# Kernel tuning notes

Hardware: AMD Instinct MI355X
Metric: run time of the kernel (lower is better)

Reference implementation:

```python
import jax, jax.numpy as jnp
import numpy as np

T, H, I, E, K = 2048, 2048, 1408, 8, 2


def setup_inputs() -> dict:
    key = jax.random.key(0)
    k1, k2, k3, k4, k5 = jax.random.split(key, 5)
    s_h = 1.0 / np.sqrt(H)
    s_i = 1.0 / np.sqrt(I)
    return {
        "hidden_states": jax.random.normal(k1, (T, H), dtype=jnp.float32),
        "router_logits": jax.random.normal(k2, (T, E), dtype=jnp.float32),
        "Wg": jax.random.normal(k3, (E, H, I), dtype=jnp.float32) * s_h,
        "Wu": jax.random.normal(k4, (E, H, I), dtype=jnp.float32) * s_h,
        "Wd": jax.random.normal(k5, (E, I, H), dtype=jnp.float32) * s_i,
        "top_k": K,
    }


def reference(hidden_states, router_logits, Wg, Wu, Wd, top_k):
    # top-k routing: softmax over the selected top-k logits (as in torch.topk + softmax)
    topk_vals, topk_ids = jax.lax.top_k(router_logits, top_k)  # [T,K]
    topk_w = jax.nn.softmax(topk_vals, axis=-1)                # [T,K]

    n_tok = hidden_states.shape[0]
    n_exp = router_logits.shape[-1]
    # combine weights [T,E]: scatter top-k weights back to expert slots
    cw = jnp.zeros((n_tok, n_exp), hidden_states.dtype)
    cw = cw.at[jnp.arange(n_tok)[:, None], topk_ids].add(topk_w)

    out = jnp.zeros_like(hidden_states)
    for e in range(n_exp):  # small fixed expert count
        g = hidden_states @ Wg[e]          # [T,I]
        u = hidden_states @ Wu[e]          # [T,I]
        y = (jax.nn.silu(g) * u) @ Wd[e]   # [T,H]
        out = out + cw[:, e:e + 1] * y
    return out
```

## Files before the change

### kernel.cpp

```cpp
#include <hip/hip_runtime.h>
#include <hip/hip_bf16.h>
#include <cstdint>
#include <cstddef>

#define TT 2048
#define HH 2048
#define II 1408
#define EE 8
#define MAXROWS 5120

typedef unsigned short u16;
typedef __attribute__((ext_vector_type(8))) __bf16 bf16x8;
typedef __attribute__((ext_vector_type(4))) float f32x4;

typedef const __attribute__((address_space(1))) uint32_t* gas1_t;
typedef __attribute__((address_space(3))) uint32_t* las3_t;

__device__ __forceinline__ float bf2f(u16 b) {
    return __uint_as_float(((uint32_t)b) << 16);
}
__device__ __forceinline__ u16 f2bf(float x) {
    uint32_t u = __float_as_uint(x);
    u += 0x7fffu + ((u >> 16) & 1u);
    return (u16)(u >> 16);
}

__global__ void k_sniff(const u16* __restrict__ raw, int* __restrict__ flag) {
    __shared__ int cnt;
    if (threadIdx.x == 0) cnt = 0;
    __syncthreads();
    int w = 0;
    for (int i = threadIdx.x; i < 4096; i += 256) {
        u16 x = raw[i];
        if (x & 0x7fff) {
            int ex = (x >> 7) & 0xff;
            if (ex == 0xff || ex < 100 || ex > 140) ++w;
        }
    }
    atomicAdd(&cnt, w);
    __syncthreads();
    if (threadIdx.x == 0) flag[0] = (cnt > 100) ? 1 : 0;
}

__global__ void k_zero(float* __restrict__ out_acc, int* __restrict__ counts) {
    const int i0 = (blockIdx.x * 256 + threadIdx.x) * 4;
    *(float4*)&out_acc[i0] = make_float4(0.f, 0.f, 0.f, 0.f);
    if (blockIdx.x == 0 && threadIdx.x < EE) counts[threadIdx.x] = 0;
}

__global__ void k_routing2(const void* __restrict__ logits, const int* __restrict__ flag,
                           int* __restrict__ counts, int* __restrict__ idx,
                           float* __restrict__ wt) {
    int t = blockIdx.x * 256 + threadIdx.x;
    if (t >= TT) return;
    const int f = flag[0];
    float v[EE];
#pragma unroll
    for (int e = 0; e < EE; ++e)
        v[e] = f ? ((const float*)logits)[t * EE + e]
                 : bf2f(((const u16*)logits)[t * EE + e]);
    int i0 = 0; float v0 = v[0];
#pragma unroll
    for (int e = 1; e < EE; ++e) { if (v[e] > v0) { v0 = v[e]; i0 = e; } }
    int i1 = -1; float v1 = -3.4e38f;
#pragma unroll
    for (int e = 0; e < EE; ++e) { if (e != i0 && v[e] > v1) { v1 = v[e]; i1 = e; } }
    float r = __expf(v1 - v0);
    float s = 1.f / (1.f + r);
    int p0 = atomicAdd(&counts[i0], 1);
    idx[i0 * TT + p0] = t; wt[i0 * TT + p0] = s;
    int p1 = atomicAdd(&counts[i1], 1);
    idx[i1 * TT + p1] = t; wt[i1 * TT + p1] = r * s;
}

__global__ void k_offsets(const int* __restrict__ counts, int* __restrict__ meta) {
    if (threadIdx.x == 0 && blockIdx.x == 0) {
        int off = 0;
        for (int e = 0; e < EE; ++e) {
            int c = counts[e];
            int p = (c + 127) & ~127;
            meta[e] = off; meta[8 + e] = p;
            off += p;
        }
    }
}

__global__ void k_cast(const void* __restrict__ src, const int* __restrict__ flag,
                       u16* __restrict__ dst) {
    const int i0 = (blockIdx.x * 256 + threadIdx.x) * 8;
    if (flag[0]) {
        const float* s = (const float*)src;
#pragma unroll
        for (int j = 0; j < 8; ++j) dst[i0 + j] = f2bf(s[i0 + j]);
    } else {
        const u16* s = (const u16*)src;
        *(uint4*)&dst[i0] = *(const uint4*)&s[i0];
    }
}

__global__ void k_transposeV(const void* __restrict__ src, const int* __restrict__ flag,
                             u16* __restrict__ dst, int R, int C) {
    __shared__ u16 t[64][68];
    const size_t eo = (size_t)blockIdx.z * (size_t)R * (size_t)C;
    const int r0 = blockIdx.y * 64, c0 = blockIdx.x * 64;
    const int tid = threadIdx.x;
    const int f = flag[0];
    {
        const int cg = tid & 15, rr = tid >> 4;
#pragma unroll
        for (int p = 0; p < 4; ++p) {
            const int r = rr + p * 16;
            const size_t base = eo + (size_t)(r0 + r) * C + c0 + cg * 4;
            if (f) {
                const float4 v = *(const float4*)((const float*)src + base);
                t[r][cg * 4 + 0] = f2bf(v.x); t[r][cg * 4 + 1] = f2bf(v.y);
                t[r][cg * 4 + 2] = f2bf(v.z); t[r][cg * 4 + 3] = f2bf(v.w);
            } else {
                const ushort4 v = *(const ushort4*)((const u16*)src + base);
                t[r][cg * 4 + 0] = v.x; t[r][cg * 4 + 1] = v.y;
                t[r][cg * 4 + 2] = v.z; t[r][cg * 4 + 3] = v.w;
            }
        }
    }
    __syncthreads();
    {
        const int rg = tid & 15, cc = tid >> 4;
#pragma unroll
        for (int p = 0; p < 4; ++p) {
            const int c = cc + p * 16;
            ushort4 o;
            o.x = t[rg * 4 + 0][c]; o.y = t[rg * 4 + 1][c];
            o.z = t[rg * 4 + 2][c]; o.w = t[rg * 4 + 3][c];
            *(ushort4*)(dst + eo + (size_t)(c0 + c) * R + r0 + rg * 4) = o;
        }
    }
}

__device__ __forceinline__ void stage16(const u16* __restrict__ g, int stride_elems,
                                        u16* lds, int wave, int lane) {
    const int sub = lane >> 2;
    const int col = (lane & 3) * 8;
#pragma unroll
    for (int h = 0; h < 2; ++h) {
        const int rbase = wave * 32 + h * 16;
        const u16* ga = g + (size_t)(rbase + sub) * stride_elems + col;
        __builtin_amdgcn_global_load_lds((gas1_t)ga, (las3_t)(lds + rbase * 32), 16, 0, 0);
    }
}

__global__ __launch_bounds__(256, 2)
void k_gemm1s(const u16* __restrict__ hs_b,
              const u16* __restrict__ Wgt,
              const u16* __restrict__ Wut,
              const int* __restrict__ counts,
              const int* __restrict__ meta,
              const int* __restrict__ idx,
              const float* __restrict__ wt,
              u16* __restrict__ act_g) {
    const int e = blockIdx.z;
    const int cnt = counts[e];
    const int pcnt = meta[8 + e];
    const int m0 = blockIdx.y * 128;
    if (m0 >= pcnt) return;
    const int n0 = blockIdx.x * 128;
    const int off = meta[e];
    const int tid = threadIdx.x;
    const int wave = tid >> 6, lane = tid & 63;
    const int ln = lane & 15, q = lane >> 4;
    const int wr = (wave >> 1) * 64, wc = (wave & 1) * 64;

    __shared__ __align__(16) u16 As[128 * 32];
    __shared__ __align__(16) u16 Bg[128 * 32];
    __shared__ __align__(16) u16 Bu[128 * 32];
    __shared__ int   tokS[128];
    __shared__ float wtS[128];

    if (tid < 128) {
        const int pos = m0 + tid;
        const bool v = pos < cnt;
        tokS[tid] = v ? idx[e * TT + pos] : 0;
        wtS[tid]  = v ? wt[e * TT + pos] : 0.f;
    }
    __syncthreads();

    const int sub = lane >> 2, col = (lane & 3) * 8;
    const int r0 = wave * 32 + sub;
    const u16* pA0 = hs_b + (size_t)tokS[r0] * HH + col;
    const u16* pA1 = hs_b + (size_t)tokS[r0 + 16] * HH + col;
    const u16* gG = Wgt + ((size_t)e * II + n0) * HH;
    const u16* gU = Wut + ((size_t)e * II + n0) * HH;

    f32x4 accg[4][4], accu[4][4];
#pragma unroll
    for (int mi = 0; mi < 4; ++mi)
#pragma unroll
        for (int ni = 0; ni < 4; ++ni) { accg[mi][ni] = (f32x4)0.f; accu[mi][ni] = (f32x4)0.f; }

    for (int kb = 0; kb < HH; kb += 32) {
        __syncthreads();
        __builtin_amdgcn_global_load_lds((gas1_t)(pA0 + kb), (las3_t)(As + (wave * 32) * 32), 16, 0, 0);
        __builtin_amdgcn_global_load_lds((gas1_t)(pA1 + kb), (las3_t)(As + (wave * 32 + 16) * 32), 16, 0, 0);
        stage16(gG + kb, HH, Bg, wave, lane);
        stage16(gU + kb, HH, Bu, wave, lane);
        __syncthreads();

        bf16x8 af[4];
#pragma unroll
        for (int mi = 0; mi < 4; ++mi)
            af[mi] = *(const bf16x8*)&As[(wr + mi * 16 + ln) * 32 + q * 8];
#pragma unroll
        for (int ni = 0; ni < 4; ++ni) {
            bf16x8 bgf = *(const bf16x8*)&Bg[(wc + ni * 16 + ln) * 32 + q * 8];
            bf16x8 buf = *(const bf16x8*)&Bu[(wc + ni * 16 + ln) * 32 + q * 8];
#pragma unroll
            for (int mi = 0; mi < 4; ++mi) {
                accg[mi][ni] = __builtin_amdgcn_mfma_f32_16x16x32_bf16(af[mi], bgf, accg[mi][ni], 0, 0, 0);
                accu[mi][ni] = __builtin_amdgcn_mfma_f32_16x16x32_bf16(af[mi], buf, accu[mi][ni], 0, 0, 0);
            }
        }
    }

#pragma unroll
    for (int mi = 0; mi < 4; ++mi) {
#pragma unroll
        for (int r = 0; r < 4; ++r) {
            const int row = wr + mi * 16 + q * 4 + r;
            const float w = wtS[row];
#pragma unroll
            for (int ni = 0; ni < 4; ++ni) {
                const int i = n0 + wc + ni * 16 + ln;
                const float g = accg[mi][ni][r];
                const float u = accu[mi][ni][r];
                const float y = w * u * g / (1.f + __expf(-g));
                act_g[(size_t)(off + m0 + row) * II + i] = f2bf(y);
            }
        }
    }
}

__global__ __launch_bounds__(256, 2)
void k_gemm2s(const u16* __restrict__ act_g,
              const u16* __restrict__ Wdt,
              const int* __restrict__ counts,
              const int* __restrict__ meta,
              const int* __restrict__ idx,
              float* __restrict__ out_acc) {
    const int e = blockIdx.z;
    const int cnt = counts[e];
    const int pcnt = meta[8 + e];
    const int m0 = blockIdx.y * 128;
    if (m0 >= pcnt) return;
    const int n0 = blockIdx.x * 128;
    const int off = meta[e];
    const int tid = threadIdx.x;
    const int wave = tid >> 6, lane = tid & 63;
    const int ln = lane & 15, q = lane >> 4;
    const int wr = (wave >> 1) * 64, wc = (wave & 1) * 64;

    __shared__ __align__(16) u16 As[128 * 32];
    __shared__ __align__(16) u16 Bs[128 * 32];
    __shared__ int tokS[128];

    if (tid < 128) {
        const int pos = m0 + tid;
        tokS[tid] = (pos < cnt) ? idx[e * TT + pos] : -1;
    }

    const u16* bA = act_g + (size_t)(off + m0) * II;
    const u16* bB = Wdt + ((size_t)e * HH + n0) * II;

    f32x4 acc[4][4];
#pragma unroll
    for (int mi = 0; mi < 4; ++mi)
#pragma unroll
        for (int ni = 0; ni < 4; ++ni) acc[mi][ni] = (f32x4)0.f;

    for (int i0 = 0; i0 < II; i0 += 32) {
        __syncthreads();
        stage16(bA + i0, II, As, wave, lane);
        stage16(bB + i0, II, Bs, wave, lane);
        __syncthreads();

        bf16x8 af[4];
#pragma unroll
        for (int mi = 0; mi < 4; ++mi)
            af[mi] = *(const bf16x8*)&As[(wr + mi * 16 + ln) * 32 + q * 8];
#pragma unroll
        for (int ni = 0; ni < 4; ++ni) {
            bf16x8 bf = *(const bf16x8*)&Bs[(wc + ni * 16 + ln) * 32 + q * 8];
#pragma unroll
            for (int mi = 0; mi < 4; ++mi)
                acc[mi][ni] = __builtin_amdgcn_mfma_f32_16x16x32_bf16(af[mi], bf, acc[mi][ni], 0, 0, 0);
        }
    }

#pragma unroll
    for (int mi = 0; mi < 4; ++mi) {
#pragma unroll
        for (int r = 0; r < 4; ++r) {
            const int row = wr + mi * 16 + q * 4 + r;
            const int t = tokS[row];
            if (t >= 0) {
#pragma unroll
                for (int ni = 0; ni < 4; ++ni) {
                    const int h = n0 + wc + ni * 16 + ln;
                    unsafeAtomicAdd(&out_acc[(size_t)t * HH + h], acc[mi][ni][r]);
                }
            }
        }
    }
}

__global__ void k_out(const float* __restrict__ out_acc, const int* __restrict__ flag,
                      void* __restrict__ out) {
    const int i0 = (blockIdx.x * 256 + threadIdx.x) * 4;
    const float4 v = *(const float4*)&out_acc[i0];
    if (flag[0]) {
        *(float4*)((float*)out + i0) = v;
    } else {
        u16* o = (u16*)out + i0;
        o[0] = f2bf(v.x); o[1] = f2bf(v.y); o[2] = f2bf(v.z); o[3] = f2bf(v.w);
    }
}

extern "C" void kernel_launch(void* const* d_in, const int* in_sizes, int n_in,
                              void* d_out, int out_size, void* d_ws, size_t ws_size,
                              hipStream_t stream) {
    (void)in_sizes; (void)n_in; (void)out_size;
    const void* hs     = d_in[0];
    const void* logits = d_in[1];
    const void* Wg     = d_in[2];
    const void* Wu     = d_in[3];
    const void* Wd     = d_in[4];

    char* ws = (char*)d_ws;
    size_t off = 0;
    int*   flag   = (int*)(ws + off);   off += 256;
    int*   counts = (int*)(ws + off);   off += 256;
    int*   meta   = (int*)(ws + off);   off += 256;
    int*   idx    = (int*)(ws + off);   off += (size_t)EE * TT * 4;
    float* wt     = (float*)(ws + off); off += (size_t)EE * TT * 4;
    u16*   hs_b   = (u16*)(ws + off);   off += (size_t)TT * HH * 2;
    u16*   Wgt    = (u16*)(ws + off);   off += (size_t)EE * II * HH * 2;
    u16*   Wut    = (u16*)(ws + off);   off += (size_t)EE * II * HH * 2;
    u16*   Wdt    = (u16*)(ws + off);   off += (size_t)EE * HH * II * 2;
    u16*   act_g  = (u16*)(ws + off);   off += (size_t)MAXROWS * II * 2;
    float* outacc = (float*)(ws + off); off += (size_t)TT * HH * 4;
    if (ws_size < off) return;

    k_sniff<<<dim3(1), dim3(256), 0, stream>>>((const u16*)hs, flag);
    k_zero<<<dim3(TT * HH / (256 * 4)), dim3(256), 0, stream>>>(outacc, counts);
    k_routing2<<<dim3(TT / 256), dim3(256), 0, stream>>>(logits, flag, counts, idx, wt);
    k_offsets<<<dim3(1), dim3(64), 0, stream>>>(counts, meta);
    k_cast<<<dim3(TT * HH / (256 * 8)), dim3(256), 0, stream>>>(hs, flag, hs_b);
    k_transposeV<<<dim3(II / 64, HH / 64, EE), dim3(256), 0, stream>>>(Wg, flag, Wgt, HH, II);
    k_transposeV<<<dim3(II / 64, HH / 64, EE), dim3(256), 0, stream>>>(Wu, flag, Wut, HH, II);
    k_transposeV<<<dim3(HH / 64, II / 64, EE), dim3(256), 0, stream>>>(Wd, flag, Wdt, II, HH);
    k_gemm1s<<<dim3(II / 128, TT / 128, EE), dim3(256), 0, stream>>>(hs_b, Wgt, Wut, counts, meta, idx, wt, act_g);
    k_gemm2s<<<dim3(HH / 128, TT / 128, EE), dim3(256), 0, stream>>>(act_g, Wdt, counts, meta, idx, outacc);
    k_out<<<dim3(TT * HH / (256 * 4)), dim3(256), 0, stream>>>(outacc, flag, d_out);
}
```

Before: 494.3 us.

## Use 512-thread blocks in gate/up GEMM and reorder grid with expert fastest

The gate/up GEMM goes from 256 to 512 threads per block, so each of 8 waves computes a 64x32 sub-tile and each thread stages one 16-byte chunk of A, Bg and Bu per k-step. Both grouped GEMMs now put the expert index in blockIdx.x, so consecutive blocks cover different experts instead of sweeping N tiles of one expert. The aim is to halve per-wave accumulator registers so more waves fit per CU, which helps hide the gather and weight-load latency. The cost is smaller per-wave tiles, which means more LDS fragment reads per MFMA. The new dispatch order may also change how well weight tiles are reused in L2.

Result: faster. 479.6 us (-3.0%).

```diff
diff --git a/kernel.cpp b/kernel.cpp
--- a/kernel.cpp
+++ b/kernel.cpp
@@ -148,7 +148,7 @@
     }
 }
 
-__global__ __launch_bounds__(256, 2)
+__global__ __launch_bounds__(512, 4)
 void k_gemm1s(const u16* __restrict__ hs_b,
               const u16* __restrict__ Wgt,
               const u16* __restrict__ Wut,
@@ -157,17 +157,18 @@
               const int* __restrict__ idx,
               const float* __restrict__ wt,
               u16* __restrict__ act_g) {
-    const int e = blockIdx.z;
+    const int e = blockIdx.x;
     const int cnt = counts[e];
     const int pcnt = meta[8 + e];
-    const int m0 = blockIdx.y * 128;
+    const int m0 = blockIdx.z * 128;
     if (m0 >= pcnt) return;
-    const int n0 = blockIdx.x * 128;
+    const int n0 = blockIdx.y * 128;
     const int off = meta[e];
     const int tid = threadIdx.x;
     const int wave = tid >> 6, lane = tid & 63;
     const int ln = lane & 15, q = lane >> 4;
-    const int wr = (wave >> 1) * 64, wc = (wave & 1) * 64;
+    const int wr = (wave >> 2) * 64;
+    const int wc = (wave & 3) * 32;
 
     __shared__ __align__(16) u16 As[128 * 32];
     __shared__ __align__(16) u16 Bg[128 * 32];
@@ -183,25 +184,26 @@
     }
     __syncthreads();
 
-    const int sub = lane >> 2, col = (lane & 3) * 8;
-    const int r0 = wave * 32 + sub;
-    const u16* pA0 = hs_b + (size_t)tokS[r0] * HH + col;
-    const u16* pA1 = hs_b + (size_t)tokS[r0 + 16] * HH + col;
-    const u16* gG = Wgt + ((size_t)e * II + n0) * HH;
-    const u16* gU = Wut + ((size_t)e * II + n0) * HH;
-
-    f32x4 accg[4][4], accu[4][4];
+    const int srow = tid >> 2;
+    const int scol = (tid & 3) * 8;
+    const u16* pA = hs_b + (size_t)tokS[srow] * HH + scol;
+    const u16* pG = Wgt + ((size_t)e * II + n0 + srow) * HH + scol;
+    const u16* pU = Wut + ((size_t)e * II + n0 + srow) * HH + scol;
+    u16* const lA = As + srow * 32 + scol;
+    u16* const lG = Bg + srow * 32 + scol;
+    u16* const lU = Bu + srow * 32 + scol;
+
+    f32x4 accg[4][2], accu[4][2];
 #pragma unroll
     for (int mi = 0; mi < 4; ++mi)
 #pragma unroll
-        for (int ni = 0; ni < 4; ++ni) { accg[mi][ni] = (f32x4)0.f; accu[mi][ni] = (f32x4)0.f; }
+        for (int ni = 0; ni < 2; ++ni) { accg[mi][ni] = (f32x4)0.f; accu[mi][ni] = (f32x4)0.f; }
 
     for (int kb = 0; kb < HH; kb += 32) {
         __syncthreads();
-        __builtin_amdgcn_global_load_lds((gas1_t)(pA0 + kb), (las3_t)(As + (wave * 32) * 32), 16, 0, 0);
-        __builtin_amdgcn_global_load_lds((gas1_t)(pA1 + kb), (las3_t)(As + (wave * 32 + 16) * 32), 16, 0, 0);
-        stage16(gG + kb, HH, Bg, wave, lane);
-        stage16(gU + kb, HH, Bu, wave, lane);
+        __builtin_amdgcn_global_load_lds((gas1_t)(pA + kb), (las3_t)lA, 16, 0, 0);
+        __builtin_amdgcn_global_load_lds((gas1_t)(pG + kb), (las3_t)lG, 16, 0, 0);
+        __builtin_amdgcn_global_load_lds((gas1_t)(pU + kb), (las3_t)lU, 16, 0, 0);
         __syncthreads();
 
         bf16x8 af[4];
@@ -209,7 +211,7 @@
         for (int mi = 0; mi < 4; ++mi)
             af[mi] = *(const bf16x8*)&As[(wr + mi * 16 + ln) * 32 + q * 8];
 #pragma unroll
-        for (int ni = 0; ni < 4; ++ni) {
+        for (int ni = 0; ni < 2; ++ni) {
             bf16x8 bgf = *(const bf16x8*)&Bg[(wc + ni * 16 + ln) * 32 + q * 8];
             bf16x8 buf = *(const bf16x8*)&Bu[(wc + ni * 16 + ln) * 32 + q * 8];
 #pragma unroll
@@ -227,7 +229,7 @@
             const int row = wr + mi * 16 + q * 4 + r;
             const float w = wtS[row];
 #pragma unroll
-            for (int ni = 0; ni < 4; ++ni) {
+            for (int ni = 0; ni < 2; ++ni) {
                 const int i = n0 + wc + ni * 16 + ln;
                 const float g = accg[mi][ni][r];
                 const float u = accu[mi][ni][r];
@@ -245,12 +247,12 @@
               const int* __restrict__ meta,
               const int* __restrict__ idx,
               float* __restrict__ out_acc) {
-    const int e = blockIdx.z;
+    const int e = blockIdx.x;
     const int cnt = counts[e];
     const int pcnt = meta[8 + e];
-    const int m0 = blockIdx.y * 128;
+    const int m0 = blockIdx.z * 128;
     if (m0 >= pcnt) return;
-    const int n0 = blockIdx.x * 128;
+    const int n0 = blockIdx.y * 128;
     const int off = meta[e];
     const int tid = threadIdx.x;
     const int wave = tid >> 6, lane = tid & 63;
@@ -356,7 +358,7 @@
     k_transposeV<<<dim3(II / 64, HH / 64, EE), dim3(256), 0, stream>>>(Wg, flag, Wgt, HH, II);
     k_transposeV<<<dim3(II / 64, HH / 64, EE), dim3(256), 0, stream>>>(Wu, flag, Wut, HH, II);
     k_transposeV<<<dim3(HH / 64, II / 64, EE), dim3(256), 0, stream>>>(Wd, flag, Wdt, II, HH);
-    k_gemm1s<<<dim3(II / 128, TT / 128, EE), dim3(256), 0, stream>>>(hs_b, Wgt, Wut, counts, meta, idx, wt, act_g);
-    k_gemm2s<<<dim3(HH / 128, TT / 128, EE), dim3(256), 0, stream>>>(act_g, Wdt, counts, meta, idx, outacc);
+    k_gemm1s<<<dim3(EE, II / 128, TT / 128), dim3(512), 0, stream>>>(hs_b, Wgt, Wut, counts, meta, idx, wt, act_g);
+    k_gemm2s<<<dim3(EE, HH / 128, TT / 128), dim3(256), 0, stream>>>(act_g, Wdt, counts, meta, idx, outacc);
     k_out<<<dim3(TT * HH / (256 * 4)), dim3(256), 0, stream>>>(outacc, flag, d_out);
 }
```
